# Optimization experiments

Measured on AMD Instinct MI355X. Metric: run time of the kernel, lower is better.

## Reference

```python
import jax, jax.numpy as jnp
import numpy as np

SR = 44100
FFT = 4096
HOP = 1024
K = FFT // 2 + 1  # 2049 bands
A_SAMP = int(10.0 * SR / 1000)    # attack_ms=10
R_SAMP = int(100.0 * SR / 1000)   # release_ms=100
A_COEFF = float(1.0 - np.exp(-1.0 / A_SAMP))
R_COEFF = float(1.0 - np.exp(-1.0 / R_SAMP))


def _lin2db(x):
    return 20.0 * jnp.log10(jnp.clip(x, 1e-8))


def _db2lin(db):
    return jnp.power(10.0, db / 20.0)


def setup_inputs() -> dict:
    key = jax.random.key(0)
    audio = jax.random.normal(key, (8, 2, 524288), dtype=jnp.float32)
    n = np.arange(FFT)
    # torch.hann_window default is periodic: 0.5*(1-cos(2*pi*n/N))
    window = jnp.asarray(0.5 * (1.0 - np.cos(2.0 * np.pi * n / FFT)), dtype=jnp.float32)
    threshold_db = jnp.full((K,), -20.0, dtype=jnp.float32)
    ratio = jnp.full((K,), 4.0, dtype=jnp.float32)
    makeup_gain_db = jnp.zeros((K,), dtype=jnp.float32)
    knee_width_db = jnp.full((K,), 6.0, dtype=jnp.float32)
    return {"audio": audio, "window": window, "threshold_db": threshold_db,
            "ratio": ratio, "makeup_gain_db": makeup_gain_db,
            "knee_width_db": knee_width_db}


def reference(audio, window, threshold_db, ratio, makeup_gain_db, knee_width_db):
    B, C, T = audio.shape
    pad = (HOP - T % HOP) % HOP  # static
    if pad > 0:
        audio = jnp.pad(audio, ((0, 0), (0, 0), (0, pad)))
    P = audio.shape[-1]
    starts = np.arange(0, P - FFT + 1, HOP)          # (F,) static
    idx = starts[:, None] + np.arange(FFT)[None, :]  # (F, FFT) static

    frames = audio[:, :, idx] * window               # (B, C, F, FFT)
    fft = jnp.fft.rfft(frames, axis=-1)              # (B, C, F, K) complex64
    mag_db = _lin2db(jnp.abs(fft))

    # soft-knee gain reduction (knee_width_db.mean() > 0 branch of original)
    knee_start = threshold_db - knee_width_db / 2
    knee_end = threshold_db + knee_width_db / 2
    over = mag_db - threshold_db
    slope = 1.0 - 1.0 / ratio
    hard = jnp.where(mag_db < threshold_db, jnp.zeros_like(mag_db), over * slope)
    kf = jnp.clip((mag_db - knee_start) / knee_width_db, 0.0, 1.0)
    knee_gain = kf * kf * over * slope
    in_knee = (mag_db >= knee_start) & (mag_db <= knee_end)
    gr_db = jnp.where(in_knee, knee_gain, hard)      # (B, C, F, K)

    # sequential attack/release envelope recurrence across frames
    def step(env, gr_t):  # env, gr_t: (B, C, K)
        tgt = _db2lin(-gr_t)
        coeff = jnp.where(tgt < env, A_COEFF, R_COEFF)
        env = env + coeff * (tgt - env)
        return env, -_lin2db(env)

    env0 = jnp.zeros((B, C, K), dtype=audio.dtype)
    _, sm = jax.lax.scan(step, env0, jnp.moveaxis(gr_db, 2, 0))  # (F, B, C, K)
    sm = jnp.moveaxis(sm, 0, 2)                      # (B, C, F, K)

    comp_mag = _db2lin(mag_db - sm + makeup_gain_db)
    cfft = comp_mag * jnp.exp(1j * jnp.angle(fft))
    ca = jnp.fft.irfft(cfft, n=FFT, axis=-1)         # (B, C, F, FFT)

    out = jnp.zeros_like(audio).at[:, :, idx].add(ca * window)  # overlap-add
    if pad > 0:
        out = out[:, :, :T]
    return out
```

## Files before the change

### kernel.cpp

```cpp
#include <hip/hip_runtime.h>
#include <hip/hip_fp16.h>

#define NFFT     4096
#define NC       2048
#define NHOP     1024
#define NK       2049
#define NBC      16
#define NSAMP    524288
#define NFRAMES  509
#define NFR2     520
#define NT       256
#define STH      64
#define SPSTR    1025
#define RSTR     1025

#define A_COEFF 0.0022650046943f
#define R_COEFF 0.00022673165872f
#define DB2LIN_LOG2 0.16609640474436812f
#define DB_LOG2     6.02059991327962390f
#define PI_D 3.14159265358979323846264338327950288

#define SW(e) ((e) + 7*((e)>>5))
#define SWSZ 2489
#define TWN  292
#define WSHDR 131072

typedef float cplx __attribute__((ext_vector_type(2)));
#define C2(a,b) ((cplx){(float)(a), (float)(b)})

__device__ __forceinline__ cplx cmul(cplx a, cplx b){
    cplx p = C2(a.x, a.x) * b;
    cplx q = C2(a.y, a.y) * C2(b.y, b.x);
    return C2(p.x - q.x, p.y + q.y);
}
__device__ __forceinline__ cplx cmulc(cplx a, cplx b){
    cplx p = C2(a.x, a.x) * b;
    cplx q = C2(a.y, a.y) * C2(b.y, b.x);
    return C2(p.x + q.x, q.y - p.y);
}

union HU { unsigned u; __half2 h; };
__device__ __forceinline__ unsigned packh2(float a, float b){
    HU x; x.h = __floats2half2_rn(a, b); return x.u;
}
__device__ __forceinline__ cplx unpackh2(unsigned v){
    HU x; x.u = v; float2 r = __half22float2(x.h); return C2(r.x, r.y);
}

#define RSQRT2 0.70710678118654752f

__device__ __forceinline__ int revm(int p){
    return (p>>8) + 8*((p>>5)&7) + 64*((p>>2)&7) + 512*(p&3);
}
__device__ __forceinline__ int pmap(int k){
    return ((k&7)<<8) | (((k>>3)&7)<<5) | (((k>>6)&7)<<2) | ((k>>9)&3);
}
__device__ __forceinline__ int p_of_m(int m){ return ((m>>1)<<2) | (m&1); }

__device__ __forceinline__ void r8f(cplx* d, const float4* __restrict__ tw12,
                                    const float2* __restrict__ tw3t, int n, int toff){
    cplx EA0=d[0]+d[4], EA1=d[0]-d[4];
    cplx EB0=d[2]+d[6], EB1=d[2]-d[6];
    cplx OA0=d[1]+d[5], OA1=d[1]-d[5];
    cplx OB0=d[3]+d[7], OB1=d[3]-d[7];
    cplx E0=EA0+EB0, E2=EA0-EB0;
    cplx E1=C2(EA1.x+EB1.y, EA1.y-EB1.x);
    cplx E3=C2(EA1.x-EB1.y, EA1.y+EB1.x);
    cplx O0=OA0+OB0, O2=OA0-OB0;
    cplx O1=C2(OA1.x+OB1.y, OA1.y-OB1.x);
    cplx O3=C2(OA1.x-OB1.y, OA1.y+OB1.x);
    const float c = RSQRT2;
    cplx t1=C2(c*(O1.x+O1.y), c*(O1.y-O1.x));
    cplx u2=C2(O2.y, -O2.x);
    cplx v3=C2(c*(O3.y-O3.x), -c*(O3.x+O3.y));
    float4 w12 = tw12[toff + n];
    cplx w1 = C2(w12.x, w12.y), w2 = C2(w12.z, w12.w);
    float2 w3l = tw3t[toff + n];
    cplx w3 = C2(w3l.x, w3l.y);
    cplx w4 = cmul(w2,w2), w5 = cmul(w2,w3), w6 = cmul(w3,w3), w7 = cmul(w3,w4);
    d[0] = E0+O0;
    d[1] = cmul(E1+t1, w1);
    d[2] = cmul(E2+u2, w2);
    d[3] = cmul(E3+v3, w3);
    d[4] = cmul(E0-O0, w4);
    d[5] = cmul(E1-t1, w5);
    d[6] = cmul(E2-u2, w6);
    d[7] = cmul(E3-v3, w7);
}

__device__ __forceinline__ void r8i(cplx* d, const float4* __restrict__ tw12,
                                    const float2* __restrict__ tw3t, int n, int toff){
    float4 w12 = tw12[toff + n];
    cplx w1 = C2(w12.x, w12.y), w2 = C2(w12.z, w12.w);
    float2 w3l = tw3t[toff + n];
    cplx w3 = C2(w3l.x, w3l.y);
    cplx w4 = cmul(w2,w2), w5 = cmul(w2,w3), w6 = cmul(w3,w3), w7 = cmul(w3,w4);
    d[1]=cmulc(d[1],w1); d[2]=cmulc(d[2],w2); d[3]=cmulc(d[3],w3); d[4]=cmulc(d[4],w4);
    d[5]=cmulc(d[5],w5); d[6]=cmulc(d[6],w6); d[7]=cmulc(d[7],w7);
    cplx EA0=d[0]+d[4], EA1=d[0]-d[4];
    cplx EB0=d[2]+d[6], EB1=d[2]-d[6];
    cplx OA0=d[1]+d[5], OA1=d[1]-d[5];
    cplx OB0=d[3]+d[7], OB1=d[3]-d[7];
    cplx E0=EA0+EB0, E2=EA0-EB0;
    cplx E1=C2(EA1.x-EB1.y, EA1.y+EB1.x);
    cplx E3=C2(EA1.x+EB1.y, EA1.y-EB1.x);
    cplx O0=OA0+OB0, O2=OA0-OB0;
    cplx O1=C2(OA1.x-OB1.y, OA1.y+OB1.x);
    cplx O3=C2(OA1.x+OB1.y, OA1.y-OB1.x);
    const float c = RSQRT2;
    cplx t1=C2(c*(O1.x-O1.y), c*(O1.y+O1.x));
    cplx u2=C2(-O2.y, O2.x);
    cplx v3=C2(-c*(O3.x+O3.y), c*(O3.x-O3.y));
    d[0] = E0+O0;
    d[1] = E1+t1;
    d[2] = E2+u2;
    d[3] = E3+v3;
    d[4] = E0-O0;
    d[5] = E1-t1;
    d[6] = E2-u2;
    d[7] = E3-v3;
}

__device__ __forceinline__ void fft_fwd_rest(cplx* s, const float4* __restrict__ tw12,
                                             const float2* __restrict__ tw3t, int tid){
    __syncthreads();
    {
        int base = (tid>>5)*256 + (tid&31);
        cplx d[8];
#pragma unroll
        for (int q = 0; q < 8; ++q) d[q] = s[SW(base + 32*q)];
        r8f(d, tw12, tw3t, tid&31, 256);
#pragma unroll
        for (int q = 0; q < 8; ++q) s[SW(base + 32*q)] = d[q];
    }
    __syncthreads();
    {
        int base = (tid>>2)*32 + (tid&3);
        cplx d[8];
#pragma unroll
        for (int q = 0; q < 8; ++q) d[q] = s[SW(base + 4*q)];
        r8f(d, tw12, tw3t, tid&3, 288);
#pragma unroll
        for (int q = 0; q < 8; ++q) s[SW(base + 4*q)] = d[q];
    }
    __syncthreads();
    {
        int g8 = 8*tid;
#pragma unroll
        for (int h = 0; h < 2; ++h) {
            int b4 = g8 + 4*h;
            cplx x0=s[SW(b4)], x1=s[SW(b4+1)], x2=s[SW(b4+2)], x3=s[SW(b4+3)];
            cplx A0=x0+x2, A1=x0-x2;
            cplx B0=x1+x3, B1=x1-x3;
            s[SW(b4)]   = A0+B0;
            s[SW(b4+1)] = C2(A1.x + B1.y, A1.y - B1.x);
            s[SW(b4+2)] = A0-B0;
            s[SW(b4+3)] = C2(A1.x - B1.y, A1.y + B1.x);
        }
    }
    __syncthreads();
}

__device__ __forceinline__ void fft_inv_rest(cplx* s, const float4* __restrict__ tw12,
                                             const float2* __restrict__ tw3t, int tid){
    {
        int g8 = 8*tid;
#pragma unroll
        for (int h = 0; h < 2; ++h) {
            int b4 = g8 + 4*h;
            cplx z0=s[SW(b4)], z1=s[SW(b4+1)], z2=s[SW(b4+2)], z3=s[SW(b4+3)];
            cplx A0=z0+z2, A1=z0-z2;
            cplx B0=z1+z3, B1=z1-z3;
            s[SW(b4)]   = A0+B0;
            s[SW(b4+1)] = C2(A1.x - B1.y, A1.y + B1.x);
            s[SW(b4+2)] = A0-B0;
            s[SW(b4+3)] = C2(A1.x + B1.y, A1.y - B1.x);
        }
    }
    __syncthreads();
    {
        int base = (tid>>2)*32 + (tid&3);
        cplx d[8];
#pragma unroll
        for (int q = 0; q < 8; ++q) d[q] = s[SW(base + 4*q)];
        r8i(d, tw12, tw3t, tid&3, 288);
#pragma unroll
        for (int q = 0; q < 8; ++q) s[SW(base + 4*q)] = d[q];
    }
    __syncthreads();
    {
        int base = (tid>>5)*256 + (tid&31);
        cplx d[8];
#pragma unroll
        for (int q = 0; q < 8; ++q) d[q] = s[SW(base + 32*q)];
        r8i(d, tw12, tw3t, tid&31, 256);
#pragma unroll
        for (int q = 0; q < 8; ++q) s[SW(base + 32*q)] = d[q];
    }
    __syncthreads();
}

__device__ __forceinline__ float gr_of2(float a2, float4 q){
    float mag_db = 0.5f * DB_LOG2 * log2f(fmaxf(a2, 1e-16f));
    float over = mag_db - q.x;
    float hard = (mag_db < q.x) ? 0.0f : over*q.w;
    float kf = fminf(fmaxf((mag_db - q.y)*q.z, 0.0f), 1.0f);
    float kneeg = kf*kf*over*q.w;
    float ke = 2.0f*q.x - q.y;
    return (mag_db >= q.y && mag_db <= ke) ? kneeg : hard;
}

__device__ __forceinline__ cplx scale_bin(cplx X, float g){
    float a2 = X.x*X.x + X.y*X.y;
    if (a2 >= 1e-16f) return C2(g,g)*X;
    if (a2 > 0.f)  { float sc = g*1e-8f*rsqrtf(a2); return C2(sc,sc)*X; }
    return C2(g*1e-8f, 0.f);
}

__global__ __launch_bounds__(NT) void k_init(
    const float* __restrict__ thr, const float* __restrict__ ratio,
    const float* __restrict__ knee, const float* __restrict__ makeup,
    float4* __restrict__ tw12, float2* __restrict__ tw3t,
    float4* __restrict__ wp, float4* __restrict__ pa, float4* __restrict__ pb,
    float2* __restrict__ mkq2)
{
    int i = blockIdx.x*NT + threadIdx.x;
    if (i < TWN) {
        int n, len;
        if (i < 256)      { n = i;       len = 2048; }
        else if (i < 288) { n = i - 256; len = 256;  }
        else              { n = i - 288; len = 32;   }
        double ang = -2.0*PI_D*(double)n/(double)len;
        tw12[i] = make_float4((float)cos(ang), (float)sin(ang),
                              (float)cos(2.0*ang), (float)sin(2.0*ang));
        tw3t[i] = make_float2((float)cos(3.0*ang), (float)sin(3.0*ang));
    } else if (i < TWN + 1024) {
        int m = i - TWN;
        int p  = p_of_m(m);
        int k  = revm(p);
        int k2 = (k == 0) ? 2048 : 2048 - k;
        int p2 = pmap((2048 - k) & 2047);
        double ang = -PI_D*(double)k/2048.0;
        wp[m] = make_float4((float)cos(ang), (float)sin(ang),
                            __int_as_float(p), __int_as_float(p2));
        float th = thr[k], ra = ratio[k], kw = knee[k];
        pa[m] = make_float4(th, th - 0.5f*kw, 1.0f/kw, 1.0f - 1.0f/ra);
        th = thr[k2]; ra = ratio[k2]; kw = knee[k2];
        pb[m] = make_float4(th, th - 0.5f*kw, 1.0f/kw, 1.0f - 1.0f/ra);
        mkq2[m] = make_float2(exp2f(makeup[k]  * DB2LIN_LOG2),
                              exp2f(makeup[k2] * DB2LIN_LOG2));
    } else if (i == TWN + 1024) {
        mkq2[1024] = make_float2(exp2f(makeup[1024] * DB2LIN_LOG2), 1.0f);
    }
}

template<int STORESPEC>
__global__ __launch_bounds__(NT, 8) void k_fwd(
    const float* __restrict__ audio, const float* __restrict__ window,
    const float* __restrict__ thr, const float* __restrict__ ratio,
    const float* __restrict__ knee,
    const float4* __restrict__ tw12, const float2* __restrict__ tw3t,
    const float4* __restrict__ wp, const float4* __restrict__ pa,
    const float4* __restrict__ pb,
    unsigned* __restrict__ gr, uint2* __restrict__ spec)
{
    __shared__ cplx s[SWSZ];
    const int tid = threadIdx.x;
    const int blk = blockIdx.x;
    const int bc  = blk / NFRAMES;
    const int f   = blk - bc*NFRAMES;

    const float2* a2c = (const float2*)(audio + (size_t)bc*NSAMP + (size_t)f*NHOP);
    const float2* w2c = (const float2*)window;
    {
        cplx d[8];
#pragma unroll
        for (int q = 0; q < 8; ++q) {
            int n = tid + 256*q;
            float2 u = a2c[n], w = w2c[n];
            d[q] = C2(u.x*w.x, u.y*w.y);
        }
        r8f(d, tw12, tw3t, tid, 0);
#pragma unroll
        for (int q = 0; q < 8; ++q) s[SW(tid + 256*q)] = d[q];
    }
    fft_fwd_rest(s, tw12, tw3t, tid);

    unsigned* grow = gr + (size_t)(bc*NFR2 + f) * RSTR;
    uint2* spx = spec + (size_t)(bc*NFRAMES + f) * SPSTR;
#pragma unroll
    for (int j = 0; j < 4; ++j) {
        int m  = tid + NT*j;
        float4 wpv = wp[m];
        int p  = __float_as_int(wpv.z);
        int p2 = __float_as_int(wpv.w);
        cplx Zk  = s[SW(p)];
        cplx Zk2 = s[SW(p2)];
        cplx Ze = C2(0.5f*(Zk.x + Zk2.x), 0.5f*(Zk.y - Zk2.y));
        cplx Zo = C2(0.5f*(Zk.y + Zk2.y), -0.5f*(Zk.x - Zk2.x));
        cplx W  = C2(wpv.x, wpv.y);
        cplx V  = cmul(W, Zo);
        cplx Xk  = Ze + V;
        cplx Xk2 = C2(Ze.x - V.x, V.y - Ze.y);
        if (STORESPEC)
            spx[m] = make_uint2(packh2(Xk.x, Xk.y), packh2(Xk2.x, Xk2.y));
        grow[m] = packh2(gr_of2(Xk.x*Xk.x + Xk.y*Xk.y,   pa[m]),
                         gr_of2(Xk2.x*Xk2.x + Xk2.y*Xk2.y, pb[m]));
    }
    if (tid == 0) {
        cplx Z = s[SW(2)];
        if (STORESPEC) spx[1024] = make_uint2(packh2(Z.x, -Z.y), 0u);
        float th = thr[1024], ra = ratio[1024], kw = knee[1024];
        float4 q = make_float4(th, th - 0.5f*kw, 1.0f/kw, 1.0f - 1.0f/ra);
        grow[1024] = packh2(gr_of2(Z.x*Z.x + Z.y*Z.y, q), 0.f);
    }
}

__device__ __forceinline__ void sm_batch8(unsigned* v, float& env1, float& env2,
                                          float2 mk, unsigned* p, int c){
    float t1[8], t2[8];
#pragma unroll
    for (int d = 0; d < 8; ++d) {
        cplx gdb = unpackh2(v[d]);
        t1[d] = exp2f(gdb.x * -DB2LIN_LOG2);
        t2[d] = exp2f(gdb.y * -DB2LIN_LOG2);
    }
#pragma unroll
    for (int d = 0; d < 8; ++d) {
        float c1 = (t1[d] < env1) ? A_COEFF : R_COEFF;
        env1 = fmaf(c1, t1[d] - env1, env1);
        float c2 = (t2[d] < env2) ? A_COEFF : R_COEFF;
        env2 = fmaf(c2, t2[d] - env2, env2);
        v[d] = packh2(fmaxf(env1, 1e-8f) * mk.x,
                      fmaxf(env2, 1e-8f) * mk.y);
    }
#pragma unroll
    for (int d = 0; d < 8; ++d) p[(size_t)(c+d)*RSTR] = v[d];
}

__global__ __launch_bounds__(STH) void k_smooth(
    unsigned* __restrict__ gr, const float2* __restrict__ mkq2)
{
    int gid = blockIdx.x*STH + threadIdx.x;
    if (gid >= NBC*RSTR) return;
    int bc = gid / RSTR;
    int m  = gid - bc*RSTR;
    float2 mk = mkq2[m];
    unsigned* p = gr + (size_t)bc*NFR2*RSTR + m;

    float env1 = 0.f, env2 = 0.f;
    unsigned b[4][8], n[4][8];
#pragma unroll
    for (int g = 0; g < 4; ++g)
#pragma unroll
        for (int d = 0; d < 8; ++d) b[g][d] = p[(size_t)(8*g + d)*RSTR];

    for (int c = 0; c < 512; c += 32) {
        if (c < 480) {
#pragma unroll
            for (int g = 0; g < 4; ++g)
#pragma unroll
                for (int d = 0; d < 8; ++d)
                    n[g][d] = p[(size_t)(c + 32 + 8*g + d)*RSTR];
        }
#pragma unroll
        for (int g = 0; g < 4; ++g)
            sm_batch8(b[g], env1, env2, mk, p, c + 8*g);
#pragma unroll
        for (int g = 0; g < 4; ++g)
#pragma unroll
            for (int d = 0; d < 8; ++d) b[g][d] = n[g][d];
    }
}

__device__ __forceinline__ void repack_pair(cplx* s, cplx XSk, cplx XSk2,
                                            cplx W, int p, int p2){
    cplx E = C2(0.5f*(XSk.x + XSk2.x), 0.5f*(XSk.y - XSk2.y));
    cplx P = C2(0.5f*(XSk.x - XSk2.x), 0.5f*(XSk.y + XSk2.y));
    cplx Wc = C2(W.x, -W.y);
    cplx Q  = cmul(Wc, P);
    cplx Pc = C2(P.x, -P.y);
    cplx R  = cmul(W, Pc);
    s[SW(p)]  = C2(E.x - Q.y, E.y + Q.x);
    s[SW(p2)] = C2(E.x - R.y, R.x - E.y);
}

template<int MODE>
__global__ __launch_bounds__(NT, 8) void k_inv(
    const float* __restrict__ audio, const float* __restrict__ window,
    const unsigned* __restrict__ gains,
    const float4* __restrict__ tw12, const float2* __restrict__ tw3t,
    const float4* __restrict__ wp,
    uint2* __restrict__ spec, float* __restrict__ out, int pass, int nfp)
{
    __shared__ cplx s[SWSZ];
    const int tid = threadIdx.x;
    const int blk = blockIdx.x;
    int bc, f;
    if (MODE != 2) { bc = blk / NFRAMES; f = blk - bc*NFRAMES; }
    else           { bc = blk / nfp;     f = pass + 4*(blk - bc*nfp); }

    const float2* w2c = (const float2*)window;
    const unsigned* grow = gains + (size_t)(bc*NFR2 + f) * RSTR;
    uint2* spx = spec + (size_t)(bc*NFRAMES + f) * SPSTR;

    if (MODE != 2) {
#pragma unroll
        for (int j = 0; j < 4; ++j) {
            int m = tid + NT*j;
            uint2 v = spx[m];
            float4 wpv = wp[m];
            cplx gg = unpackh2(grow[m]);
            cplx XSk  = scale_bin(unpackh2(v.x), gg.x);
            cplx XSk2 = scale_bin(unpackh2(v.y), gg.y);
            repack_pair(s, XSk, XSk2, C2(wpv.x, wpv.y),
                        __float_as_int(wpv.z), __float_as_int(wpv.w));
        }
        if (tid == 0) {
            uint2 v = spx[1024];
            cplx gg = unpackh2(grow[1024]);
            cplx XS = scale_bin(unpackh2(v.x), gg.x);
            s[SW(2)] = C2(XS.x, -XS.y);
        }
        __syncthreads();
    } else {
        {
            const float2* a2c = (const float2*)(audio + (size_t)bc*NSAMP + (size_t)f*NHOP);
            cplx d[8];
#pragma unroll
            for (int q = 0; q < 8; ++q) {
                int n = tid + 256*q;
                float2 u = a2c[n], w = w2c[n];
                d[q] = C2(u.x*w.x, u.y*w.y);
            }
            r8f(d, tw12, tw3t, tid, 0);
#pragma unroll
            for (int q = 0; q < 8; ++q) s[SW(tid + 256*q)] = d[q];
        }
        fft_fwd_rest(s, tw12, tw3t, tid);
#pragma unroll
        for (int j = 0; j < 4; ++j) {
            int m = tid + NT*j;
            float4 wpv = wp[m];
            int p  = __float_as_int(wpv.z);
            int p2 = __float_as_int(wpv.w);
            cplx Zk  = s[SW(p)];
            cplx Zk2 = s[SW(p2)];
            cplx Ze = C2(0.5f*(Zk.x + Zk2.x), 0.5f*(Zk.y - Zk2.y));
            cplx Zo = C2(0.5f*(Zk.y + Zk2.y), -0.5f*(Zk.x - Zk2.x));
            cplx W  = C2(wpv.x, wpv.y);
            cplx V  = cmul(W, Zo);
            cplx Xk  = Ze + V;
            cplx Xk2 = C2(Ze.x - V.x, V.y - Ze.y);
            cplx gg = unpackh2(grow[m]);
            cplx XSk  = scale_bin(Xk,  gg.x);
            cplx XSk2 = scale_bin(Xk2, gg.y);
            repack_pair(s, XSk, XSk2, W, p, p2);
        }
        if (tid == 0) {
            cplx Z  = s[SW(2)];
            cplx gg = unpackh2(grow[1024]);
            cplx XS = scale_bin(C2(Z.x, -Z.y), gg.x);
            s[SW(2)] = C2(XS.x, -XS.y);
        }
        __syncthreads();
    }

    fft_inv_rest(s, tw12, tw3t, tid);

    const float invn = 1.0f/2048.0f;
    {
        cplx d[8];
#pragma unroll
        for (int q = 0; q < 8; ++q) d[q] = s[SW(tid + 256*q)];
        r8i(d, tw12, tw3t, tid, 0);
        if (MODE == 1) {
            unsigned* caH = (unsigned*)spx;
#pragma unroll
            for (int q = 0; q < 8; ++q) {
                int n = tid + 256*q;
                float2 w = w2c[n];
                caH[n] = packh2(d[q].x*w.x*invn, d[q].y*w.y*invn);
            }
        } else {
            float2* dst2 = (float2*)(out + (size_t)bc*NSAMP + (size_t)f*NHOP);
#pragma unroll
            for (int q = 0; q < 8; ++q) {
                int n = tid + 256*q;
                float2 w = w2c[n];
                float2 o = dst2[n];
                o.x += d[q].x * w.x * invn;
                o.y += d[q].y * w.y * invn;
                dst2[n] = o;
            }
        }
    }
}

__global__ __launch_bounds__(NT) void k_ola(
    const uint2* __restrict__ spec, float* __restrict__ out)
{
    const int blk = blockIdx.x;
    const int bc = blk >> 9;
    const int ti = blk & 511;
    const int tid = threadIdx.x;
    float4 acc = make_float4(0.f, 0.f, 0.f, 0.f);
    int flo = ti - 3; if (flo < 0) flo = 0;
    int fhi = ti; if (fhi > NFRAMES - 1) fhi = NFRAMES - 1;
    for (int f = flo; f <= fhi; ++f) {
        const uint2* row = spec + (size_t)(bc*NFRAMES + f) * SPSTR;
        uint2 v = row[(ti - f)*256 + tid];
        cplx a = unpackh2(v.x), b = unpackh2(v.y);
        acc.x += a.x; acc.y += a.y; acc.z += b.x; acc.w += b.y;
    }
    ((float4*)(out + (size_t)bc*NSAMP))[ti*256 + tid] = acc;
}

extern "C" void kernel_launch(void* const* d_in, const int* in_sizes, int n_in,
                              void* d_out, int out_size, void* d_ws, size_t ws_size,
                              hipStream_t stream)
{
    const float* audio  = (const float*)d_in[0];
    const float* window = (const float*)d_in[1];
    const float* thr    = (const float*)d_in[2];
    const float* ratio  = (const float*)d_in[3];
    const float* makeup = (const float*)d_in[4];
    const float* knee   = (const float*)d_in[5];
    float* out = (float*)d_out;

    char* base = (char*)d_ws;
    float4* tw12 = (float4*)base;
    float2* tw3t = (float2*)(base + 8192);
    float4* wp   = (float4*)(base + 16384);
    float4* pa   = (float4*)(base + 32768);
    float4* pb   = (float4*)(base + 49152);
    float2* mkq2 = (float2*)(base + 65536);
    unsigned* gr = (unsigned*)(base + WSHDR);
    const size_t grB = (size_t)NBC*NFR2*RSTR*sizeof(unsigned);
    const size_t spB = (size_t)NBC*NFRAMES*SPSTR*sizeof(uint2);
    const size_t needB = WSHDR + grB + spB;

    dim3 blkd(NT);
    k_init<<<dim3((TWN + 1025 + NT - 1)/NT), blkd, 0, stream>>>(
        thr, ratio, knee, makeup, tw12, tw3t, wp, pa, pb, mkq2);

    int sblocks = (NBC*RSTR + STH - 1)/STH;
    if (ws_size >= needB) {
        uint2* spec = (uint2*)(base + WSHDR + grB);
        k_fwd<1><<<dim3(NBC*NFRAMES), blkd, 0, stream>>>(
            audio, window, thr, ratio, knee, tw12, tw3t, wp, pa, pb, gr, spec);
        k_smooth<<<dim3(sblocks), dim3(STH), 0, stream>>>(gr, mkq2);
        k_inv<1><<<dim3(NBC*NFRAMES), blkd, 0, stream>>>(
            audio, window, gr, tw12, tw3t, wp, spec, out, 0, 0);
        k_ola<<<dim3(NBC*512), blkd, 0, stream>>>(spec, out);
    } else {
        hipMemsetAsync(d_out, 0, (size_t)out_size*sizeof(float), stream);
        uint2* spec = (uint2*)(base + WSHDR + grB);
        k_fwd<0><<<dim3(NBC*NFRAMES), blkd, 0, stream>>>(
            audio, window, thr, ratio, knee, tw12, tw3t, wp, pa, pb, gr, spec);
        k_smooth<<<dim3(sblocks), dim3(STH), 0, stream>>>(gr, mkq2);
        for (int pass = 0; pass < 4; ++pass) {
            int nfp = (NFRAMES - pass + 3) / 4;
            k_inv<2><<<dim3(NBC*nfp), blkd, 0, stream>>>(
                audio, window, gr, tw12, tw3t, wp, spec, out, pass, nfp);
        }
    }
}
```

Baseline: 168.6 us.

## Process two frames per block in forward and inverse FFT kernels

The forward and inverse FFT kernels now handle two adjacent frames per 256-thread block. Twiddle loads and their derived products are shared between both frames, and each thread gets twice the independent work for latency hiding. Blocks are also remapped with an XCD-style swizzle (blockIdx interleaved by 8) in the fwd, inv and OLA kernels to improve L2 locality on the multi-die GPU. This doubles the shared memory per block and lowers launch bounds occupancy from 8 to 4, which may reduce concurrency.

```diff
diff --git a/kernel.cpp b/kernel.cpp
--- a/kernel.cpp
+++ b/kernel.cpp
@@ -13,6 +13,7 @@
 #define STH      64
 #define SPSTR    1025
 #define RSTR     1025
+#define PPC      255
 
 #define A_COEFF 0.0022650046943f
 #define R_COEFF 0.00022673165872f
@@ -25,6 +26,8 @@
 #define TWN  292
 #define WSHDR 131072
 
+__device__ __forceinline__ int xswz(int b, int cpx){ return (b & 7)*cpx + (b >> 3); }
+
 typedef float cplx __attribute__((ext_vector_type(2)));
 #define C2(a,b) ((cplx){(float)(a), (float)(b)})
 
@@ -57,8 +60,20 @@
 }
 __device__ __forceinline__ int p_of_m(int m){ return ((m>>1)<<2) | (m&1); }
 
-__device__ __forceinline__ void r8f(cplx* d, const float4* __restrict__ tw12,
-                                    const float2* __restrict__ tw3t, int n, int toff){
+struct TwSet { cplx w1,w2,w3,w4,w5,w6,w7; };
+__device__ __forceinline__ TwSet twload(const float4* __restrict__ tw12,
+                                        const float2* __restrict__ tw3t, int n, int toff){
+    TwSet t;
+    float4 w12 = tw12[toff + n];
+    t.w1 = C2(w12.x, w12.y); t.w2 = C2(w12.z, w12.w);
+    float2 w3l = tw3t[toff + n];
+    t.w3 = C2(w3l.x, w3l.y);
+    t.w4 = cmul(t.w2,t.w2); t.w5 = cmul(t.w2,t.w3);
+    t.w6 = cmul(t.w3,t.w3); t.w7 = cmul(t.w3,t.w4);
+    return t;
+}
+
+__device__ __forceinline__ void r8f_core(cplx* d, const TwSet& t){
     cplx EA0=d[0]+d[4], EA1=d[0]-d[4];
     cplx EB0=d[2]+d[6], EB1=d[2]-d[6];
     cplx OA0=d[1]+d[5], OA1=d[1]-d[5];
@@ -73,30 +88,19 @@
     cplx t1=C2(c*(O1.x+O1.y), c*(O1.y-O1.x));
     cplx u2=C2(O2.y, -O2.x);
     cplx v3=C2(c*(O3.y-O3.x), -c*(O3.x+O3.y));
-    float4 w12 = tw12[toff + n];
-    cplx w1 = C2(w12.x, w12.y), w2 = C2(w12.z, w12.w);
-    float2 w3l = tw3t[toff + n];
-    cplx w3 = C2(w3l.x, w3l.y);
-    cplx w4 = cmul(w2,w2), w5 = cmul(w2,w3), w6 = cmul(w3,w3), w7 = cmul(w3,w4);
     d[0] = E0+O0;
-    d[1] = cmul(E1+t1, w1);
-    d[2] = cmul(E2+u2, w2);
-    d[3] = cmul(E3+v3, w3);
-    d[4] = cmul(E0-O0, w4);
-    d[5] = cmul(E1-t1, w5);
-    d[6] = cmul(E2-u2, w6);
-    d[7] = cmul(E3-v3, w7);
-}
-
-__device__ __forceinline__ void r8i(cplx* d, const float4* __restrict__ tw12,
-                                    const float2* __restrict__ tw3t, int n, int toff){
-    float4 w12 = tw12[toff + n];
-    cplx w1 = C2(w12.x, w12.y), w2 = C2(w12.z, w12.w);
-    float2 w3l = tw3t[toff + n];
-    cplx w3 = C2(w3l.x, w3l.y);
-    cplx w4 = cmul(w2,w2), w5 = cmul(w2,w3), w6 = cmul(w3,w3), w7 = cmul(w3,w4);
-    d[1]=cmulc(d[1],w1); d[2]=cmulc(d[2],w2); d[3]=cmulc(d[3],w3); d[4]=cmulc(d[4],w4);
-    d[5]=cmulc(d[5],w5); d[6]=cmulc(d[6],w6); d[7]=cmulc(d[7],w7);
+    d[1] = cmul(E1+t1, t.w1);
+    d[2] = cmul(E2+u2, t.w2);
+    d[3] = cmul(E3+v3, t.w3);
+    d[4] = cmul(E0-O0, t.w4);
+    d[5] = cmul(E1-t1, t.w5);
+    d[6] = cmul(E2-u2, t.w6);
+    d[7] = cmul(E3-v3, t.w7);
+}
+
+__device__ __forceinline__ void r8i_core(cplx* d, const TwSet& t){
+    d[1]=cmulc(d[1],t.w1); d[2]=cmulc(d[2],t.w2); d[3]=cmulc(d[3],t.w3); d[4]=cmulc(d[4],t.w4);
+    d[5]=cmulc(d[5],t.w5); d[6]=cmulc(d[6],t.w6); d[7]=cmulc(d[7],t.w7);
     cplx EA0=d[0]+d[4], EA1=d[0]-d[4];
     cplx EB0=d[2]+d[6], EB1=d[2]-d[6];
     cplx OA0=d[1]+d[5], OA1=d[1]-d[5];
@@ -111,41 +115,121 @@
     cplx t1=C2(c*(O1.x-O1.y), c*(O1.y+O1.x));
     cplx u2=C2(-O2.y, O2.x);
     cplx v3=C2(-c*(O3.x+O3.y), c*(O3.x-O3.y));
-    d[0] = E0+O0;
-    d[1] = E1+t1;
-    d[2] = E2+u2;
-    d[3] = E3+v3;
-    d[4] = E0-O0;
-    d[5] = E1-t1;
-    d[6] = E2-u2;
-    d[7] = E3-v3;
+    d[0] = E0+O0; d[1] = E1+t1; d[2] = E2+u2; d[3] = E3+v3;
+    d[4] = E0-O0; d[5] = E1-t1; d[6] = E2-u2; d[7] = E3-v3;
+}
+
+__device__ __forceinline__ void fft_fwd_rest2(cplx* s0, cplx* s1,
+                                              const float4* __restrict__ tw12,
+                                              const float2* __restrict__ tw3t, int tid){
+    __syncthreads();
+    {
+        int base = (tid>>5)*256 + (tid&31);
+        cplx d0[8], d1[8];
+#pragma unroll
+        for (int q = 0; q < 8; ++q) { d0[q] = s0[SW(base + 32*q)]; d1[q] = s1[SW(base + 32*q)]; }
+        TwSet t = twload(tw12, tw3t, tid&31, 256);
+        r8f_core(d0, t); r8f_core(d1, t);
+#pragma unroll
+        for (int q = 0; q < 8; ++q) { s0[SW(base + 32*q)] = d0[q]; s1[SW(base + 32*q)] = d1[q]; }
+    }
+    __syncthreads();
+    {
+        int base = (tid>>2)*32 + (tid&3);
+        cplx d0[8], d1[8];
+#pragma unroll
+        for (int q = 0; q < 8; ++q) { d0[q] = s0[SW(base + 4*q)]; d1[q] = s1[SW(base + 4*q)]; }
+        TwSet t = twload(tw12, tw3t, tid&3, 288);
+        r8f_core(d0, t); r8f_core(d1, t);
+#pragma unroll
+        for (int q = 0; q < 8; ++q) { s0[SW(base + 4*q)] = d0[q]; s1[SW(base + 4*q)] = d1[q]; }
+    }
+    __syncthreads();
+    {
+        int g8 = 8*tid;
+#pragma unroll
+        for (int h = 0; h < 4; ++h) {
+            cplx* s = (h & 1) ? s1 : s0;
+            int b4 = g8 + 4*(h>>1);
+            cplx x0=s[SW(b4)], x1=s[SW(b4+1)], x2=s[SW(b4+2)], x3=s[SW(b4+3)];
+            cplx A0=x0+x2, A1=x0-x2;
+            cplx B0=x1+x3, B1=x1-x3;
+            s[SW(b4)]   = A0+B0;
+            s[SW(b4+1)] = C2(A1.x + B1.y, A1.y - B1.x);
+            s[SW(b4+2)] = A0-B0;
+            s[SW(b4+3)] = C2(A1.x - B1.y, A1.y + B1.x);
+        }
+    }
+    __syncthreads();
+}
+
+__device__ __forceinline__ void fft_inv_rest2(cplx* s0, cplx* s1,
+                                              const float4* __restrict__ tw12,
+                                              const float2* __restrict__ tw3t, int tid){
+    {
+        int g8 = 8*tid;
+#pragma unroll
+        for (int h = 0; h < 4; ++h) {
+            cplx* s = (h & 1) ? s1 : s0;
+            int b4 = g8 + 4*(h>>1);
+            cplx z0=s[SW(b4)], z1=s[SW(b4+1)], z2=s[SW(b4+2)], z3=s[SW(b4+3)];
+            cplx A0=z0+z2, A1=z0-z2;
+            cplx B0=z1+z3, B1=z1-z3;
+            s[SW(b4)]   = A0+B0;
+            s[SW(b4+1)] = C2(A1.x - B1.y, A1.y + B1.x);
+            s[SW(b4+2)] = A0-B0;
+            s[SW(b4+3)] = C2(A1.x + B1.y, A1.y - B1.x);
+        }
+    }
+    __syncthreads();
+    {
+        int base = (tid>>2)*32 + (tid&3);
+        cplx d0[8], d1[8];
+#pragma unroll
+        for (int q = 0; q < 8; ++q) { d0[q] = s0[SW(base + 4*q)]; d1[q] = s1[SW(base + 4*q)]; }
+        TwSet t = twload(tw12, tw3t, tid&3, 288);
+        r8i_core(d0, t); r8i_core(d1, t);
+#pragma unroll
+        for (int q = 0; q < 8; ++q) { s0[SW(base + 4*q)] = d0[q]; s1[SW(base + 4*q)] = d1[q]; }
+    }
+    __syncthreads();
+    {
+        int base = (tid>>5)*256 + (tid&31);
+        cplx d0[8], d1[8];
+#pragma unroll
+        for (int q = 0; q < 8; ++q) { d0[q] = s0[SW(base + 32*q)]; d1[q] = s1[SW(base + 32*q)]; }
+        TwSet t = twload(tw12, tw3t, tid&31, 256);
+        r8i_core(d0, t); r8i_core(d1, t);
+#pragma unroll
+        for (int q = 0; q < 8; ++q) { s0[SW(base + 32*q)] = d0[q]; s1[SW(base + 32*q)] = d1[q]; }
+    }
+    __syncthreads();
 }
 
 __device__ __forceinline__ void fft_fwd_rest(cplx* s, const float4* __restrict__ tw12,
                                              const float2* __restrict__ tw3t, int tid){
     __syncthreads();
-    {
-        int base = (tid>>5)*256 + (tid&31);
+    {   int base = (tid>>5)*256 + (tid&31);
         cplx d[8];
 #pragma unroll
         for (int q = 0; q < 8; ++q) d[q] = s[SW(base + 32*q)];
-        r8f(d, tw12, tw3t, tid&31, 256);
+        TwSet t = twload(tw12, tw3t, tid&31, 256);
+        r8f_core(d, t);
 #pragma unroll
         for (int q = 0; q < 8; ++q) s[SW(base + 32*q)] = d[q];
     }
     __syncthreads();
-    {
-        int base = (tid>>2)*32 + (tid&3);
+    {   int base = (tid>>2)*32 + (tid&3);
         cplx d[8];
 #pragma unroll
         for (int q = 0; q < 8; ++q) d[q] = s[SW(base + 4*q)];
-        r8f(d, tw12, tw3t, tid&3, 288);
+        TwSet t = twload(tw12, tw3t, tid&3, 288);
+        r8f_core(d, t);
 #pragma unroll
         for (int q = 0; q < 8; ++q) s[SW(base + 4*q)] = d[q];
     }
     __syncthreads();
-    {
-        int g8 = 8*tid;
+    {   int g8 = 8*tid;
 #pragma unroll
         for (int h = 0; h < 2; ++h) {
             int b4 = g8 + 4*h;
@@ -163,8 +247,7 @@
 
 __device__ __forceinline__ void fft_inv_rest(cplx* s, const float4* __restrict__ tw12,
                                              const float2* __restrict__ tw3t, int tid){
-    {
-        int g8 = 8*tid;
+    {   int g8 = 8*tid;
 #pragma unroll
         for (int h = 0; h < 2; ++h) {
             int b4 = g8 + 4*h;
@@ -178,22 +261,22 @@
         }
     }
     __syncthreads();
-    {
-        int base = (tid>>2)*32 + (tid&3);
+    {   int base = (tid>>2)*32 + (tid&3);
         cplx d[8];
 #pragma unroll
         for (int q = 0; q < 8; ++q) d[q] = s[SW(base + 4*q)];
-        r8i(d, tw12, tw3t, tid&3, 288);
+        TwSet t = twload(tw12, tw3t, tid&3, 288);
+        r8i_core(d, t);
 #pragma unroll
         for (int q = 0; q < 8; ++q) s[SW(base + 4*q)] = d[q];
     }
     __syncthreads();
-    {
-        int base = (tid>>5)*256 + (tid&31);
+    {   int base = (tid>>5)*256 + (tid&31);
         cplx d[8];
 #pragma unroll
         for (int q = 0; q < 8; ++q) d[q] = s[SW(base + 32*q)];
-        r8i(d, tw12, tw3t, tid&31, 256);
+        TwSet t = twload(tw12, tw3t, tid&31, 256);
+        r8i_core(d, t);
 #pragma unroll
         for (int q = 0; q < 8; ++q) s[SW(base + 32*q)] = d[q];
     }
@@ -254,8 +337,7 @@
     }
 }
 
-template<int STORESPEC>
-__global__ __launch_bounds__(NT, 8) void k_fwd(
+__global__ __launch_bounds__(NT, 4) void k_fwd2(
     const float* __restrict__ audio, const float* __restrict__ window,
     const float* __restrict__ thr, const float* __restrict__ ratio,
     const float* __restrict__ knee,
@@ -264,6 +346,88 @@
     const float4* __restrict__ pb,
     unsigned* __restrict__ gr, uint2* __restrict__ spec)
 {
+    __shared__ cplx s[2][SWSZ];
+    const int tid = threadIdx.x;
+    const int blk = xswz(blockIdx.x, (NBC*PPC)/8);
+    const int bc  = blk / PPC;
+    const int t2  = blk - bc*PPC;
+    const int f0  = 2*t2;
+    const int v1  = (f0 + 1 < NFRAMES);
+
+    const float2* a0 = (const float2*)(audio + (size_t)bc*NSAMP + (size_t)f0*NHOP);
+    const float2* a1 = v1 ? (a0 + 512) : a0;
+    const float2* w2c = (const float2*)window;
+    {
+        cplx d0[8], d1[8];
+#pragma unroll
+        for (int q = 0; q < 8; ++q) {
+            int n = tid + 256*q;
+            float2 w = w2c[n];
+            float2 u0 = a0[n], u1 = a1[n];
+            d0[q] = C2(u0.x*w.x, u0.y*w.y);
+            d1[q] = C2(u1.x*w.x, u1.y*w.y);
+        }
+        TwSet t = twload(tw12, tw3t, tid, 0);
+        r8f_core(d0, t); r8f_core(d1, t);
+#pragma unroll
+        for (int q = 0; q < 8; ++q) { s[0][SW(tid + 256*q)] = d0[q]; s[1][SW(tid + 256*q)] = d1[q]; }
+    }
+    fft_fwd_rest2(s[0], s[1], tw12, tw3t, tid);
+
+    unsigned* grow0 = gr + (size_t)(bc*NFR2 + f0) * RSTR;
+    unsigned* grow1 = grow0 + RSTR;
+    uint2* spx0 = spec + (size_t)(bc*NFRAMES + f0) * SPSTR;
+    uint2* spx1 = spx0 + SPSTR;
+#pragma unroll
+    for (int j = 0; j < 4; ++j) {
+        int m  = tid + NT*j;
+        float4 wpv = wp[m];
+        float4 qa = pa[m], qb = pb[m];
+        int p  = __float_as_int(wpv.z);
+        int p2 = __float_as_int(wpv.w);
+        cplx W = C2(wpv.x, wpv.y);
+#pragma unroll
+        for (int h = 0; h < 2; ++h) {
+            cplx Zk  = s[h][SW(p)];
+            cplx Zk2 = s[h][SW(p2)];
+            cplx Ze = C2(0.5f*(Zk.x + Zk2.x), 0.5f*(Zk.y - Zk2.y));
+            cplx Zo = C2(0.5f*(Zk.y + Zk2.y), -0.5f*(Zk.x - Zk2.x));
+            cplx V  = cmul(W, Zo);
+            cplx Xk  = Ze + V;
+            cplx Xk2 = C2(Ze.x - V.x, V.y - Ze.y);
+            if (h == 0) {
+                spx0[m] = make_uint2(packh2(Xk.x, Xk.y), packh2(Xk2.x, Xk2.y));
+                grow0[m] = packh2(gr_of2(Xk.x*Xk.x + Xk.y*Xk.y, qa),
+                                  gr_of2(Xk2.x*Xk2.x + Xk2.y*Xk2.y, qb));
+            } else if (v1) {
+                spx1[m] = make_uint2(packh2(Xk.x, Xk.y), packh2(Xk2.x, Xk2.y));
+                grow1[m] = packh2(gr_of2(Xk.x*Xk.x + Xk.y*Xk.y, qa),
+                                  gr_of2(Xk2.x*Xk2.x + Xk2.y*Xk2.y, qb));
+            }
+        }
+    }
+    if (tid == 0) {
+        float th = thr[1024], ra = ratio[1024], kw = knee[1024];
+        float4 q = make_float4(th, th - 0.5f*kw, 1.0f/kw, 1.0f - 1.0f/ra);
+        cplx Z0 = s[0][SW(2)];
+        spx0[1024] = make_uint2(packh2(Z0.x, -Z0.y), 0u);
+        grow0[1024] = packh2(gr_of2(Z0.x*Z0.x + Z0.y*Z0.y, q), 0.f);
+        if (v1) {
+            cplx Z1 = s[1][SW(2)];
+            spx1[1024] = make_uint2(packh2(Z1.x, -Z1.y), 0u);
+            grow1[1024] = packh2(gr_of2(Z1.x*Z1.x + Z1.y*Z1.y, q), 0.f);
+        }
+    }
+}
+
+__global__ __launch_bounds__(NT, 8) void k_fwd1(
+    const float* __restrict__ audio, const float* __restrict__ window,
+    const float* __restrict__ thr, const float* __restrict__ ratio,
+    const float* __restrict__ knee,
+    const float4* __restrict__ tw12, const float2* __restrict__ tw3t,
+    const float4* __restrict__ wp, const float4* __restrict__ pa,
+    const float4* __restrict__ pb, unsigned* __restrict__ gr)
+{
     __shared__ cplx s[SWSZ];
     const int tid = threadIdx.x;
     const int blk = blockIdx.x;
@@ -280,14 +444,14 @@
             float2 u = a2c[n], w = w2c[n];
             d[q] = C2(u.x*w.x, u.y*w.y);
         }
-        r8f(d, tw12, tw3t, tid, 0);
+        TwSet t = twload(tw12, tw3t, tid, 0);
+        r8f_core(d, t);
 #pragma unroll
         for (int q = 0; q < 8; ++q) s[SW(tid + 256*q)] = d[q];
     }
     fft_fwd_rest(s, tw12, tw3t, tid);
 
     unsigned* grow = gr + (size_t)(bc*NFR2 + f) * RSTR;
-    uint2* spx = spec + (size_t)(bc*NFRAMES + f) * SPSTR;
 #pragma unroll
     for (int j = 0; j < 4; ++j) {
         int m  = tid + NT*j;
@@ -302,14 +466,11 @@
         cplx V  = cmul(W, Zo);
         cplx Xk  = Ze + V;
         cplx Xk2 = C2(Ze.x - V.x, V.y - Ze.y);
-        if (STORESPEC)
-            spx[m] = make_uint2(packh2(Xk.x, Xk.y), packh2(Xk2.x, Xk2.y));
         grow[m] = packh2(gr_of2(Xk.x*Xk.x + Xk.y*Xk.y,   pa[m]),
                          gr_of2(Xk2.x*Xk2.x + Xk2.y*Xk2.y, pb[m]));
     }
     if (tid == 0) {
         cplx Z = s[SW(2)];
-        if (STORESPEC) spx[1024] = make_uint2(packh2(Z.x, -Z.y), 0u);
         float th = thr[1024], ra = ratio[1024], kw = knee[1024];
         float4 q = make_float4(th, th - 0.5f*kw, 1.0f/kw, 1.0f - 1.0f/ra);
         grow[1024] = packh2(gr_of2(Z.x*Z.x + Z.y*Z.y, q), 0.f);
@@ -385,122 +546,148 @@
     s[SW(p2)] = C2(E.x - R.y, R.x - E.y);
 }
 
-template<int MODE>
-__global__ __launch_bounds__(NT, 8) void k_inv(
+__global__ __launch_bounds__(NT, 4) void k_inv2(
+    const float* __restrict__ window, const unsigned* __restrict__ gains,
+    const float4* __restrict__ tw12, const float2* __restrict__ tw3t,
+    const float4* __restrict__ wp, uint2* __restrict__ spec)
+{
+    __shared__ cplx s[2][SWSZ];
+    const int tid = threadIdx.x;
+    const int blk = xswz(blockIdx.x, (NBC*PPC)/8);
+    const int bc  = blk / PPC;
+    const int t2  = blk - bc*PPC;
+    const int f0  = 2*t2;
+    const int v1  = (f0 + 1 < NFRAMES);
+
+    const float2* w2c = (const float2*)window;
+    const unsigned* grow0 = gains + (size_t)(bc*NFR2 + f0) * RSTR;
+    const unsigned* grow1 = v1 ? (grow0 + RSTR) : grow0;
+    uint2* spx0 = spec + (size_t)(bc*NFRAMES + f0) * SPSTR;
+    uint2* spx1 = v1 ? (spx0 + SPSTR) : spx0;
+
+#pragma unroll
+    for (int j = 0; j < 4; ++j) {
+        int m = tid + NT*j;
+        float4 wpv = wp[m];
+        int p  = __float_as_int(wpv.z);
+        int p2 = __float_as_int(wpv.w);
+        cplx W = C2(wpv.x, wpv.y);
+        uint2 va = spx0[m], vb = spx1[m];
+        cplx g0 = unpackh2(grow0[m]), g1 = unpackh2(grow1[m]);
+        repack_pair(s[0], scale_bin(unpackh2(va.x), g0.x),
+                          scale_bin(unpackh2(va.y), g0.y), W, p, p2);
+        repack_pair(s[1], scale_bin(unpackh2(vb.x), g1.x),
+                          scale_bin(unpackh2(vb.y), g1.y), W, p, p2);
+    }
+    if (tid == 0) {
+        uint2 va = spx0[1024], vb = spx1[1024];
+        cplx g0 = unpackh2(grow0[1024]), g1 = unpackh2(grow1[1024]);
+        cplx X0 = scale_bin(unpackh2(va.x), g0.x);
+        cplx X1 = scale_bin(unpackh2(vb.x), g1.x);
+        s[0][SW(2)] = C2(X0.x, -X0.y);
+        s[1][SW(2)] = C2(X1.x, -X1.y);
+    }
+    __syncthreads();
+
+    fft_inv_rest2(s[0], s[1], tw12, tw3t, tid);
+
+    const float invn = 1.0f/2048.0f;
+    {
+        cplx d0[8], d1[8];
+#pragma unroll
+        for (int q = 0; q < 8; ++q) { d0[q] = s[0][SW(tid + 256*q)]; d1[q] = s[1][SW(tid + 256*q)]; }
+        TwSet t = twload(tw12, tw3t, tid, 0);
+        r8i_core(d0, t); r8i_core(d1, t);
+        unsigned* ca0 = (unsigned*)spx0;
+        unsigned* ca1 = (unsigned*)spx1;
+#pragma unroll
+        for (int q = 0; q < 8; ++q) {
+            int n = tid + 256*q;
+            float2 w = w2c[n];
+            ca0[n] = packh2(d0[q].x*w.x*invn, d0[q].y*w.y*invn);
+            if (v1) ca1[n] = packh2(d1[q].x*w.x*invn, d1[q].y*w.y*invn);
+        }
+    }
+}
+
+__global__ __launch_bounds__(NT, 8) void k_inv_fb(
     const float* __restrict__ audio, const float* __restrict__ window,
     const unsigned* __restrict__ gains,
     const float4* __restrict__ tw12, const float2* __restrict__ tw3t,
-    const float4* __restrict__ wp,
-    uint2* __restrict__ spec, float* __restrict__ out, int pass, int nfp)
+    const float4* __restrict__ wp, float* __restrict__ out, int pass, int nfp)
 {
     __shared__ cplx s[SWSZ];
     const int tid = threadIdx.x;
     const int blk = blockIdx.x;
-    int bc, f;
-    if (MODE != 2) { bc = blk / NFRAMES; f = blk - bc*NFRAMES; }
-    else           { bc = blk / nfp;     f = pass + 4*(blk - bc*nfp); }
+    int bc = blk / nfp;
+    int f  = pass + 4*(blk - bc*nfp);
 
     const float2* w2c = (const float2*)window;
     const unsigned* grow = gains + (size_t)(bc*NFR2 + f) * RSTR;
-    uint2* spx = spec + (size_t)(bc*NFRAMES + f) * SPSTR;
-
-    if (MODE != 2) {
-#pragma unroll
-        for (int j = 0; j < 4; ++j) {
-            int m = tid + NT*j;
-            uint2 v = spx[m];
-            float4 wpv = wp[m];
-            cplx gg = unpackh2(grow[m]);
-            cplx XSk  = scale_bin(unpackh2(v.x), gg.x);
-            cplx XSk2 = scale_bin(unpackh2(v.y), gg.y);
-            repack_pair(s, XSk, XSk2, C2(wpv.x, wpv.y),
-                        __float_as_int(wpv.z), __float_as_int(wpv.w));
-        }
-        if (tid == 0) {
-            uint2 v = spx[1024];
-            cplx gg = unpackh2(grow[1024]);
-            cplx XS = scale_bin(unpackh2(v.x), gg.x);
-            s[SW(2)] = C2(XS.x, -XS.y);
-        }
-        __syncthreads();
-    } else {
-        {
-            const float2* a2c = (const float2*)(audio + (size_t)bc*NSAMP + (size_t)f*NHOP);
-            cplx d[8];
-#pragma unroll
-            for (int q = 0; q < 8; ++q) {
-                int n = tid + 256*q;
-                float2 u = a2c[n], w = w2c[n];
-                d[q] = C2(u.x*w.x, u.y*w.y);
-            }
-            r8f(d, tw12, tw3t, tid, 0);
-#pragma unroll
-            for (int q = 0; q < 8; ++q) s[SW(tid + 256*q)] = d[q];
-        }
-        fft_fwd_rest(s, tw12, tw3t, tid);
-#pragma unroll
-        for (int j = 0; j < 4; ++j) {
-            int m = tid + NT*j;
-            float4 wpv = wp[m];
-            int p  = __float_as_int(wpv.z);
-            int p2 = __float_as_int(wpv.w);
-            cplx Zk  = s[SW(p)];
-            cplx Zk2 = s[SW(p2)];
-            cplx Ze = C2(0.5f*(Zk.x + Zk2.x), 0.5f*(Zk.y - Zk2.y));
-            cplx Zo = C2(0.5f*(Zk.y + Zk2.y), -0.5f*(Zk.x - Zk2.x));
-            cplx W  = C2(wpv.x, wpv.y);
-            cplx V  = cmul(W, Zo);
-            cplx Xk  = Ze + V;
-            cplx Xk2 = C2(Ze.x - V.x, V.y - Ze.y);
-            cplx gg = unpackh2(grow[m]);
-            cplx XSk  = scale_bin(Xk,  gg.x);
-            cplx XSk2 = scale_bin(Xk2, gg.y);
-            repack_pair(s, XSk, XSk2, W, p, p2);
-        }
-        if (tid == 0) {
-            cplx Z  = s[SW(2)];
-            cplx gg = unpackh2(grow[1024]);
-            cplx XS = scale_bin(C2(Z.x, -Z.y), gg.x);
-            s[SW(2)] = C2(XS.x, -XS.y);
-        }
-        __syncthreads();
-    }
-
+
+    {
+        const float2* a2c = (const float2*)(audio + (size_t)bc*NSAMP + (size_t)f*NHOP);
+        cplx d[8];
+#pragma unroll
+        for (int q = 0; q < 8; ++q) {
+            int n = tid + 256*q;
+            float2 u = a2c[n], w = w2c[n];
+            d[q] = C2(u.x*w.x, u.y*w.y);
+        }
+        TwSet t = twload(tw12, tw3t, tid, 0);
+        r8f_core(d, t);
+#pragma unroll
+        for (int q = 0; q < 8; ++q) s[SW(tid + 256*q)] = d[q];
+    }
+    fft_fwd_rest(s, tw12, tw3t, tid);
+#pragma unroll
+    for (int j = 0; j < 4; ++j) {
+        int m = tid + NT*j;
+        float4 wpv = wp[m];
+        int p  = __float_as_int(wpv.z);
+        int p2 = __float_as_int(wpv.w);
+        cplx Zk  = s[SW(p)];
+        cplx Zk2 = s[SW(p2)];
+        cplx Ze = C2(0.5f*(Zk.x + Zk2.x), 0.5f*(Zk.y - Zk2.y));
+        cplx Zo = C2(0.5f*(Zk.y + Zk2.y), -0.5f*(Zk.x - Zk2.x));
+        cplx W  = C2(wpv.x, wpv.y);
+        cplx V  = cmul(W, Zo);
+        cplx Xk  = Ze + V;
+        cplx Xk2 = C2(Ze.x - V.x, V.y - Ze.y);
+        cplx gg = unpackh2(grow[m]);
+        repack_pair(s, scale_bin(Xk, gg.x), scale_bin(Xk2, gg.y), W, p, p2);
+    }
+    if (tid == 0) {
+        cplx Z  = s[SW(2)];
+        cplx gg = unpackh2(grow[1024]);
+        cplx XS = scale_bin(C2(Z.x, -Z.y), gg.x);
+        s[SW(2)] = C2(XS.x, -XS.y);
+    }
+    __syncthreads();
     fft_inv_rest(s, tw12, tw3t, tid);
 
     const float invn = 1.0f/2048.0f;
-    {
-        cplx d[8];
-#pragma unroll
-        for (int q = 0; q < 8; ++q) d[q] = s[SW(tid + 256*q)];
-        r8i(d, tw12, tw3t, tid, 0);
-        if (MODE == 1) {
-            unsigned* caH = (unsigned*)spx;
-#pragma unroll
-            for (int q = 0; q < 8; ++q) {
-                int n = tid + 256*q;
-                float2 w = w2c[n];
-                caH[n] = packh2(d[q].x*w.x*invn, d[q].y*w.y*invn);
-            }
-        } else {
-            float2* dst2 = (float2*)(out + (size_t)bc*NSAMP + (size_t)f*NHOP);
-#pragma unroll
-            for (int q = 0; q < 8; ++q) {
-                int n = tid + 256*q;
-                float2 w = w2c[n];
-                float2 o = dst2[n];
-                o.x += d[q].x * w.x * invn;
-                o.y += d[q].y * w.y * invn;
-                dst2[n] = o;
-            }
-        }
+    cplx d[8];
+#pragma unroll
+    for (int q = 0; q < 8; ++q) d[q] = s[SW(tid + 256*q)];
+    TwSet t = twload(tw12, tw3t, tid, 0);
+    r8i_core(d, t);
+    float2* dst2 = (float2*)(out + (size_t)bc*NSAMP + (size_t)f*NHOP);
+#pragma unroll
+    for (int q = 0; q < 8; ++q) {
+        int n = tid + 256*q;
+        float2 w = w2c[n];
+        float2 o = dst2[n];
+        o.x += d[q].x * w.x * invn;
+        o.y += d[q].y * w.y * invn;
+        dst2[n] = o;
     }
 }
 
 __global__ __launch_bounds__(NT) void k_ola(
     const uint2* __restrict__ spec, float* __restrict__ out)
 {
-    const int blk = blockIdx.x;
+    const int blk = xswz(blockIdx.x, (NBC*512)/8);
     const int bc = blk >> 9;
     const int ti = blk & 511;
     const int tid = threadIdx.x;
@@ -547,22 +734,21 @@
     int sblocks = (NBC*RSTR + STH - 1)/STH;
     if (ws_size >= needB) {
         uint2* spec = (uint2*)(base + WSHDR + grB);
-        k_fwd<1><<<dim3(NBC*NFRAMES), blkd, 0, stream>>>(
+        k_fwd2<<<dim3(NBC*PPC), blkd, 0, stream>>>(
             audio, window, thr, ratio, knee, tw12, tw3t, wp, pa, pb, gr, spec);
         k_smooth<<<dim3(sblocks), dim3(STH), 0, stream>>>(gr, mkq2);
-        k_inv<1><<<dim3(NBC*NFRAMES), blkd, 0, stream>>>(
-            audio, window, gr, tw12, tw3t, wp, spec, out, 0, 0);
+        k_inv2<<<dim3(NBC*PPC), blkd, 0, stream>>>(
+            window, gr, tw12, tw3t, wp, spec);
         k_ola<<<dim3(NBC*512), blkd, 0, stream>>>(spec, out);
     } else {
         hipMemsetAsync(d_out, 0, (size_t)out_size*sizeof(float), stream);
-        uint2* spec = (uint2*)(base + WSHDR + grB);
-        k_fwd<0><<<dim3(NBC*NFRAMES), blkd, 0, stream>>>(
-            audio, window, thr, ratio, knee, tw12, tw3t, wp, pa, pb, gr, spec);
+        k_fwd1<<<dim3(NBC*NFRAMES), blkd, 0, stream>>>(
+            audio, window, thr, ratio, knee, tw12, tw3t, wp, pa, pb, gr);
         k_smooth<<<dim3(sblocks), dim3(STH), 0, stream>>>(gr, mkq2);
         for (int pass = 0; pass < 4; ++pass) {
             int nfp = (NFRAMES - pass + 3) / 4;
-            k_inv<2><<<dim3(NBC*nfp), blkd, 0, stream>>>(
-                audio, window, gr, tw12, tw3t, wp, spec, out, pass, nfp);
-        }
-    }
-}
+            k_inv_fb<<<dim3(NBC*nfp), blkd, 0, stream>>>(
+                audio, window, gr, tw12, tw3t, wp, out, pass, nfp);
+        }
+    }
+}
```

Result: no change. 169.0 us (+0.3%).
